# Performance work log

Hardware: AMD Instinct MI355X
Metric: run time of the kernel (lower is better)

The kernel has to match this reference:

```python
import jax, jax.numpy as jnp
import numpy as np

N_NODES = 10000
N_EDGES = 320000
IN_DIM = 128
HIDDEN = 256
NUM_LAYERS = 6
ALPHA = 0.1
LN_EPS = 1e-5


def setup_inputs() -> dict:
    key = jax.random.key(0)
    ks = jax.random.split(key, 12)
    x = jax.random.normal(ks[0], (N_NODES, IN_DIM), dtype=jnp.float32)
    edge_index = jax.random.randint(ks[1], (2, N_EDGES), 0, N_NODES, dtype=jnp.int64)
    # input MLP params
    W_in = jax.random.normal(ks[2], (IN_DIM, HIDDEN), dtype=jnp.float32) / np.sqrt(IN_DIM)
    b_in = jnp.zeros((HIDDEN,), dtype=jnp.float32)
    g_in = jnp.ones((HIDDEN,), dtype=jnp.float32)
    beta_in = jnp.zeros((HIDDEN,), dtype=jnp.float32)
    # per-layer GCNConv weight/bias + LayerNorm params, stacked over layers
    Wl = jax.random.normal(ks[3], (NUM_LAYERS, HIDDEN, HIDDEN), dtype=jnp.float32) / np.sqrt(HIDDEN)
    bl = jnp.zeros((NUM_LAYERS, HIDDEN), dtype=jnp.float32)
    gl = jnp.ones((NUM_LAYERS, HIDDEN), dtype=jnp.float32)
    betal = jnp.zeros((NUM_LAYERS, HIDDEN), dtype=jnp.float32)
    return {"x": x, "edge_index": edge_index, "W_in": W_in, "b_in": b_in,
            "g_in": g_in, "beta_in": beta_in, "Wl": Wl, "bl": bl,
            "gl": gl, "betal": betal}


def _layernorm(h, g, b):
    mu = jnp.mean(h, axis=-1, keepdims=True)
    var = jnp.var(h, axis=-1, keepdims=True)
    return (h - mu) * jax.lax.rsqrt(var + LN_EPS) * g + b


def reference(x, edge_index, W_in, b_in, g_in, beta_in, Wl, bl, gl, betal):
    N = x.shape[0]
    # input block: Linear -> GELU (exact erf) -> LayerNorm (dropout = eval identity)
    h = jax.nn.gelu(x @ W_in + b_in, approximate=False)
    h = _layernorm(h, g_in, beta_in)

    # GCN normalization with self loops, unit edge weights (edge_weight=None)
    loops = jnp.arange(N, dtype=edge_index.dtype)
    src = jnp.concatenate([edge_index[0], loops])  # [E+N] sources (j)
    dst = jnp.concatenate([edge_index[1], loops])  # [E+N] targets (i)
    w = jnp.ones((src.shape[0],), dtype=x.dtype)
    deg = jax.ops.segment_sum(w, dst, num_segments=N)
    dinv = jnp.where(deg > 0, deg ** -0.5, 0.0)
    norm = dinv[src] * w * dinv[dst]  # [E+N]

    h0 = h
    cur = h
    for l in range(NUM_LAYERS):
        m = cur @ Wl[l]                                        # [N,H] transform
        msgs = norm[:, None] * m[src]                          # gather + scale
        agg = jax.ops.segment_sum(msgs, dst, num_segments=N)   # scatter-add
        agg = agg + bl[l]
        hh = _layernorm(jax.nn.gelu(agg, approximate=False), gl[l], betal[l])
        cur = cur + (1.0 - ALPHA) * hh + ALPHA * h0
    return cur
```

## Files before the change

### kernel.cpp

```cpp
#include <hip/hip_runtime.h>
#include <math.h>

#define N_NODES   10000
#define N_EDGES   320000
#define IN_DIM    128
#define HIDDEN    256
#define NUM_LAYERS 6
#define ALPHA     0.1f
#define LN_EPS    1e-5f

__device__ __forceinline__ float gelu_exact(float x) {
    return 0.5f * x * (1.0f + erff(x * 0.70710678118654752440f));
}

__device__ __forceinline__ float wave_sum64(float v) {
#pragma unroll
    for (int i = 32; i > 0; i >>= 1) v += __shfl_xor(v, i);
    return v;
}


__global__ __launch_bounds__(256) void count_deg_kernel(const int* __restrict__ dst,
                                                        int* __restrict__ cnt) {
    int e = blockIdx.x * 256 + threadIdx.x;
    if (e < N_EDGES) atomicAdd(&cnt[dst[e]], 1);
}

__global__ __launch_bounds__(256) void dinv_kernel(const int* __restrict__ cnt,
                                                   float* __restrict__ dinv) {
    int i = blockIdx.x * 256 + threadIdx.x;
    if (i < N_NODES) dinv[i] = rsqrtf((float)(cnt[i] + 1));
}

__global__ __launch_bounds__(256) void scan_kernel(const int* __restrict__ cnt,
                                                   int* __restrict__ offs) {
    __shared__ int sums[256];
    __shared__ int bases[257];
    int t = threadIdx.x;
    const int chunk = (N_NODES + 255) / 256;
    int b0 = t * chunk;
    int b1 = b0 + chunk; if (b1 > N_NODES) b1 = N_NODES;
    if (b0 > N_NODES) b0 = N_NODES;
    int s = 0;
    for (int i = b0; i < b1; ++i) s += cnt[i];
    sums[t] = s;
    __syncthreads();
    if (t == 0) {
        int r = 0;
        for (int i = 0; i < 256; ++i) { bases[i] = r; r += sums[i]; }
        bases[256] = r;
    }
    __syncthreads();
    int r = bases[t];
    for (int i = b0; i < b1; ++i) { offs[i] = r; r += cnt[i]; }
    if (t == 0) offs[N_NODES] = bases[256];
}

__global__ __launch_bounds__(256) void fill_csr_kernel(const int* __restrict__ src,
                                                       const int* __restrict__ dst,
                                                       const float* __restrict__ dinv,
                                                       const int* __restrict__ offs,
                                                       int* __restrict__ cursor,
                                                       int* __restrict__ csr_src,
                                                       float* __restrict__ csr_norm) {
    int e = blockIdx.x * 256 + threadIdx.x;
    if (e < N_EDGES) {
        int d = dst[e], s = src[e];
        int pos = atomicAdd(&cursor[d], 1);
        int idx = offs[d] + pos;
        csr_src[idx]  = s;
        csr_norm[idx] = dinv[s] * dinv[d];
    }
}

template<int K>
__global__ __launch_bounds__(256) void gemm_kernel(const float* __restrict__ A,
                                                   const float* __restrict__ B,
                                                   float* __restrict__ C) {
    __shared__ float As[16][68];
    __shared__ float Bs[16][68];

    int tid = threadIdx.x;
    int tx = tid & 15;
    int ty = tid >> 4;
    int row0 = blockIdx.x * 64;
    int col0 = blockIdx.y * 64;

    float acc[4][4] = {};

    for (int k0 = 0; k0 < K; k0 += 16) {
        {
            int idx = tid * 4;
            int r  = idx >> 4;
            int kk = idx & 15;
            int row = row0 + r;
            if (row < N_NODES) {
                const float4 a4 = *(const float4*)&A[(size_t)row * K + k0 + kk];
                As[kk + 0][r] = a4.x; As[kk + 1][r] = a4.y;
                As[kk + 2][r] = a4.z; As[kk + 3][r] = a4.w;
            } else {
                As[kk + 0][r] = 0.f; As[kk + 1][r] = 0.f;
                As[kk + 2][r] = 0.f; As[kk + 3][r] = 0.f;
            }
        }
        {
            int idx = tid * 4;
            int rb = idx >> 6;
            int cb = idx & 63;
            const float4 b4 = *(const float4*)&B[(size_t)(k0 + rb) * HIDDEN + col0 + cb];
            *(float4*)&Bs[rb][cb] = b4;
        }
        __syncthreads();

        #pragma unroll
        for (int kk = 0; kk < 16; ++kk) {
            const float4 a4 = *(const float4*)&As[kk][ty * 4];
            const float4 b4 = *(const float4*)&Bs[kk][tx * 4];
            acc[0][0] += a4.x * b4.x; acc[0][1] += a4.x * b4.y; acc[0][2] += a4.x * b4.z; acc[0][3] += a4.x * b4.w;
            acc[1][0] += a4.y * b4.x; acc[1][1] += a4.y * b4.y; acc[1][2] += a4.y * b4.z; acc[1][3] += a4.y * b4.w;
            acc[2][0] += a4.z * b4.x; acc[2][1] += a4.z * b4.y; acc[2][2] += a4.z * b4.z; acc[2][3] += a4.z * b4.w;
            acc[3][0] += a4.w * b4.x; acc[3][1] += a4.w * b4.y; acc[3][2] += a4.w * b4.z; acc[3][3] += a4.w * b4.w;
        }
        __syncthreads();
    }

    #pragma unroll
    for (int i = 0; i < 4; ++i) {
        int row = row0 + ty * 4 + i;
        if (row < N_NODES) {
            float4 v = make_float4(acc[i][0], acc[i][1], acc[i][2], acc[i][3]);
            *(float4*)&C[(size_t)row * HIDDEN + col0 + tx * 4] = v;
        }
    }
}

__global__ __launch_bounds__(256) void ln_in_kernel(const float4* __restrict__ pre,
                                                    const float4* __restrict__ b4,
                                                    const float4* __restrict__ g4,
                                                    const float4* __restrict__ beta4,
                                                    float4* __restrict__ h0,
                                                    float4* __restrict__ cur) {
    int n = blockIdx.x * 4 + (threadIdx.x >> 6);
    int lane = threadIdx.x & 63;
    if (n >= N_NODES) return;

    float4 v = pre[(size_t)n * 64 + lane];
    float4 bb = b4[lane];
    float x0 = gelu_exact(v.x + bb.x);
    float x1 = gelu_exact(v.y + bb.y);
    float x2 = gelu_exact(v.z + bb.z);
    float x3 = gelu_exact(v.w + bb.w);

    float mu = wave_sum64(x0 + x1 + x2 + x3) * (1.0f / 256.0f);
    float d0 = x0 - mu, d1 = x1 - mu, d2 = x2 - mu, d3 = x3 - mu;
    float var = wave_sum64(d0 * d0 + d1 * d1 + d2 * d2 + d3 * d3) * (1.0f / 256.0f);
    float r = rsqrtf(var + LN_EPS);

    float4 gg = g4[lane], be = beta4[lane];
    float4 out = make_float4(d0 * r * gg.x + be.x, d1 * r * gg.y + be.y,
                             d2 * r * gg.z + be.z, d3 * r * gg.w + be.w);
    h0[(size_t)n * 64 + lane]  = out;
    cur[(size_t)n * 64 + lane] = out;
}

__global__ __launch_bounds__(256) void agg_fused_kernel(const float4* __restrict__ m4,
                                                        const float* __restrict__ dinv,
                                                        const int* __restrict__ offs,
                                                        const int* __restrict__ csr_src,
                                                        const float* __restrict__ csr_norm,
                                                        const float4* __restrict__ bias4,
                                                        const float4* __restrict__ g4,
                                                        const float4* __restrict__ beta4,
                                                        const float4* __restrict__ h04,
                                                        float4* __restrict__ cur4) {
    int n = blockIdx.x * 4 + (threadIdx.x >> 6);
    int lane = threadIdx.x & 63;
    if (n >= N_NODES) return;

    float dn = dinv[n];
    float dn2 = dn * dn;
    float4 sv = m4[(size_t)n * 64 + lane];
    float ax = sv.x * dn2, ay = sv.y * dn2, az = sv.z * dn2, aw = sv.w * dn2;

    int e  = offs[n];
    int e1 = offs[n + 1];
    for (; e + 7 < e1; e += 8) {
        int   s0 = csr_src[e + 0], s1 = csr_src[e + 1], s2 = csr_src[e + 2], s3 = csr_src[e + 3];
        int   s4 = csr_src[e + 4], s5 = csr_src[e + 5], s6 = csr_src[e + 6], s7 = csr_src[e + 7];
        float w0 = csr_norm[e + 0], w1 = csr_norm[e + 1], w2 = csr_norm[e + 2], w3 = csr_norm[e + 3];
        float w4 = csr_norm[e + 4], w5 = csr_norm[e + 5], w6 = csr_norm[e + 6], w7 = csr_norm[e + 7];
        float4 v0 = m4[(size_t)s0 * 64 + lane];
        float4 v1 = m4[(size_t)s1 * 64 + lane];
        float4 v2 = m4[(size_t)s2 * 64 + lane];
        float4 v3 = m4[(size_t)s3 * 64 + lane];
        float4 v4 = m4[(size_t)s4 * 64 + lane];
        float4 v5 = m4[(size_t)s5 * 64 + lane];
        float4 v6 = m4[(size_t)s6 * 64 + lane];
        float4 v7 = m4[(size_t)s7 * 64 + lane];
        ax += w0 * v0.x + w1 * v1.x + w2 * v2.x + w3 * v3.x;
        ay += w0 * v0.y + w1 * v1.y + w2 * v2.y + w3 * v3.y;
        az += w0 * v0.z + w1 * v1.z + w2 * v2.z + w3 * v3.z;
        aw += w0 * v0.w + w1 * v1.w + w2 * v2.w + w3 * v3.w;
        ax += w4 * v4.x + w5 * v5.x + w6 * v6.x + w7 * v7.x;
        ay += w4 * v4.y + w5 * v5.y + w6 * v6.y + w7 * v7.y;
        az += w4 * v4.z + w5 * v5.z + w6 * v6.z + w7 * v7.z;
        aw += w4 * v4.w + w5 * v5.w + w6 * v6.w + w7 * v7.w;
    }
    for (; e < e1; ++e) {
        int s = csr_src[e];
        float w = csr_norm[e];
        float4 vv = m4[(size_t)s * 64 + lane];
        ax += w * vv.x; ay += w * vv.y; az += w * vv.z; aw += w * vv.w;
    }

    float4 bb = bias4[lane];
    float x0 = gelu_exact(ax + bb.x);
    float x1 = gelu_exact(ay + bb.y);
    float x2 = gelu_exact(az + bb.z);
    float x3 = gelu_exact(aw + bb.w);

    float mu = wave_sum64(x0 + x1 + x2 + x3) * (1.0f / 256.0f);
    float d0 = x0 - mu, d1 = x1 - mu, d2 = x2 - mu, d3 = x3 - mu;
    float var = wave_sum64(d0 * d0 + d1 * d1 + d2 * d2 + d3 * d3) * (1.0f / 256.0f);
    float r = rsqrtf(var + LN_EPS);

    float4 gg = g4[lane], be = beta4[lane];
    float h0v = d0 * r * gg.x + be.x;
    float h1v = d1 * r * gg.y + be.y;
    float h2v = d2 * r * gg.z + be.z;
    float h3v = d3 * r * gg.w + be.w;

    size_t idx = (size_t)n * 64 + lane;
    float4 c = cur4[idx];
    float4 h = h04[idx];
    float4 o = make_float4(c.x + (1.0f - ALPHA) * h0v + ALPHA * h.x,
                           c.y + (1.0f - ALPHA) * h1v + ALPHA * h.y,
                           c.z + (1.0f - ALPHA) * h2v + ALPHA * h.z,
                           c.w + (1.0f - ALPHA) * h3v + ALPHA * h.w);
    cur4[idx] = o;
}


extern "C" void kernel_launch(void* const* d_in, const int* in_sizes, int n_in,
                              void* d_out, int out_size, void* d_ws, size_t ws_size,
                              hipStream_t stream) {
    const float* x      = (const float*)d_in[0];
    const int*   ei     = (const int*)  d_in[1];
    const float* W_in   = (const float*)d_in[2];
    const float* b_in   = (const float*)d_in[3];
    const float* g_in   = (const float*)d_in[4];
    const float* bt_in  = (const float*)d_in[5];
    const float* Wl     = (const float*)d_in[6];
    const float* bl     = (const float*)d_in[7];
    const float* gl     = (const float*)d_in[8];
    const float* betal  = (const float*)d_in[9];

    const int* src = ei;
    const int* dst = ei + N_EDGES;

    float* cur = (float*)d_out;

    char* w = (char*)d_ws;
    size_t off = 0;
    auto alloc = [&](size_t bytes) -> void* {
        void* p = w + off;
        off = (off + bytes + 255) & ~(size_t)255;
        return p;
    };
    int*   cnt      = (int*)  alloc(N_NODES * sizeof(int));
    int*   cursor   = (int*)  alloc(N_NODES * sizeof(int));
    int*   offs     = (int*)  alloc((N_NODES + 1) * sizeof(int));
    float* dinv     = (float*)alloc(N_NODES * sizeof(float));
    int*   csr_src  = (int*)  alloc(N_EDGES * sizeof(int));
    float* csr_norm = (float*)alloc(N_EDGES * sizeof(float));
    float* h0       = (float*)alloc((size_t)N_NODES * HIDDEN * sizeof(float));
    float* m        = (float*)alloc((size_t)N_NODES * HIDDEN * sizeof(float));

    hipMemsetAsync(cnt,    0, N_NODES * sizeof(int), stream);
    hipMemsetAsync(cursor, 0, N_NODES * sizeof(int), stream);

    const int EB = (N_EDGES + 255) / 256;
    const int NB = (N_NODES + 255) / 256;
    const int NODE_BLOCKS = (N_NODES + 3) / 4;

    count_deg_kernel<<<EB, 256, 0, stream>>>(dst, cnt);
    dinv_kernel<<<NB, 256, 0, stream>>>(cnt, dinv);
    scan_kernel<<<1, 256, 0, stream>>>(cnt, offs);
    fill_csr_kernel<<<EB, 256, 0, stream>>>(src, dst, dinv, offs, cursor, csr_src, csr_norm);

    dim3 ggrid((N_NODES + 63) / 64, HIDDEN / 64);

    gemm_kernel<IN_DIM><<<ggrid, 256, 0, stream>>>(x, W_in, m);
    ln_in_kernel<<<NODE_BLOCKS, 256, 0, stream>>>((const float4*)m, (const float4*)b_in,
                                                  (const float4*)g_in, (const float4*)bt_in,
                                                  (float4*)h0, (float4*)cur);

    for (int l = 0; l < NUM_LAYERS; ++l) {
        gemm_kernel<HIDDEN><<<ggrid, 256, 0, stream>>>(cur, Wl + (size_t)l * HIDDEN * HIDDEN, m);
        agg_fused_kernel<<<NODE_BLOCKS, 256, 0, stream>>>((const float4*)m, dinv, offs,
                                                          csr_src, csr_norm,
                                                          (const float4*)(bl + l * HIDDEN),
                                                          (const float4*)(gl + l * HIDDEN),
                                                          (const float4*)(betal + l * HIDDEN),
                                                          (const float4*)h0, (float4*)cur);
    }
}
```

Measured before the change: 558.6 us.

## Split aggregation into column-quarter gather kernel plus separate LN-residual kernel

New measurement: 578.9 us. 1.04x slower.

```diff
diff --git a/kernel.cpp b/kernel.cpp
--- a/kernel.cpp
+++ b/kernel.cpp
@@ -58,18 +58,14 @@
 
 __global__ __launch_bounds__(256) void fill_csr_kernel(const int* __restrict__ src,
                                                        const int* __restrict__ dst,
-                                                       const float* __restrict__ dinv,
                                                        const int* __restrict__ offs,
                                                        int* __restrict__ cursor,
-                                                       int* __restrict__ csr_src,
-                                                       float* __restrict__ csr_norm) {
+                                                       int* __restrict__ csr_src) {
     int e = blockIdx.x * 256 + threadIdx.x;
     if (e < N_EDGES) {
         int d = dst[e], s = src[e];
         int pos = atomicAdd(&cursor[d], 1);
-        int idx = offs[d] + pos;
-        csr_src[idx]  = s;
-        csr_norm[idx] = dinv[s] * dinv[d];
+        csr_src[offs[d] + pos] = s;
     }
 }
 
@@ -163,61 +159,62 @@
     cur[(size_t)n * 64 + lane] = out;
 }
 
-__global__ __launch_bounds__(256) void agg_fused_kernel(const float4* __restrict__ m4,
-                                                        const float* __restrict__ dinv,
-                                                        const int* __restrict__ offs,
-                                                        const int* __restrict__ csr_src,
-                                                        const float* __restrict__ csr_norm,
-                                                        const float4* __restrict__ bias4,
-                                                        const float4* __restrict__ g4,
-                                                        const float4* __restrict__ beta4,
-                                                        const float4* __restrict__ h04,
-                                                        float4* __restrict__ cur4) {
+__global__ __launch_bounds__(256) void gather_q_kernel(const float* __restrict__ m,
+                                                       const float* __restrict__ dinv,
+                                                       const int* __restrict__ offs,
+                                                       const int* __restrict__ csr_src,
+                                                       const float* __restrict__ bias,
+                                                       float* __restrict__ pre) {
+    int i  = blockIdx.x;
+    int q  = (i & 7) >> 1;
+    int nb = (i >> 3) * 2 + (i & 1);
+    int n  = nb * 4 + (threadIdx.x >> 6);
+    int lane = threadIdx.x & 63;
+    int col = q * 64 + lane;
+
+    float dn = dinv[n];
+    float acc = m[(size_t)n * HIDDEN + col] * (dn * dn);
+
+    int e  = offs[n];
+    int e1 = offs[n + 1];
+    for (; e + 7 < e1; e += 8) {
+        int s0 = csr_src[e + 0], s1 = csr_src[e + 1], s2 = csr_src[e + 2], s3 = csr_src[e + 3];
+        int s4 = csr_src[e + 4], s5 = csr_src[e + 5], s6 = csr_src[e + 6], s7 = csr_src[e + 7];
+        float v0 = m[(size_t)s0 * HIDDEN + col];
+        float v1 = m[(size_t)s1 * HIDDEN + col];
+        float v2 = m[(size_t)s2 * HIDDEN + col];
+        float v3 = m[(size_t)s3 * HIDDEN + col];
+        float v4 = m[(size_t)s4 * HIDDEN + col];
+        float v5 = m[(size_t)s5 * HIDDEN + col];
+        float v6 = m[(size_t)s6 * HIDDEN + col];
+        float v7 = m[(size_t)s7 * HIDDEN + col];
+        float w0 = dinv[s0] * dn, w1 = dinv[s1] * dn, w2 = dinv[s2] * dn, w3 = dinv[s3] * dn;
+        float w4 = dinv[s4] * dn, w5 = dinv[s5] * dn, w6 = dinv[s6] * dn, w7 = dinv[s7] * dn;
+        acc += w0 * v0 + w1 * v1 + w2 * v2 + w3 * v3;
+        acc += w4 * v4 + w5 * v5 + w6 * v6 + w7 * v7;
+    }
+    for (; e < e1; ++e) {
+        int s = csr_src[e];
+        acc += dinv[s] * dn * m[(size_t)s * HIDDEN + col];
+    }
+
+    pre[(size_t)n * HIDDEN + col] = acc + bias[col];
+}
+
+__global__ __launch_bounds__(256) void ln_res_kernel(const float4* __restrict__ pre4,
+                                                     const float4* __restrict__ g4,
+                                                     const float4* __restrict__ beta4,
+                                                     const float4* __restrict__ h04,
+                                                     float4* __restrict__ cur4) {
     int n = blockIdx.x * 4 + (threadIdx.x >> 6);
     int lane = threadIdx.x & 63;
     if (n >= N_NODES) return;
 
-    float dn = dinv[n];
-    float dn2 = dn * dn;
-    float4 sv = m4[(size_t)n * 64 + lane];
-    float ax = sv.x * dn2, ay = sv.y * dn2, az = sv.z * dn2, aw = sv.w * dn2;
-
-    int e  = offs[n];
-    int e1 = offs[n + 1];
-    for (; e + 7 < e1; e += 8) {
-        int   s0 = csr_src[e + 0], s1 = csr_src[e + 1], s2 = csr_src[e + 2], s3 = csr_src[e + 3];
-        int   s4 = csr_src[e + 4], s5 = csr_src[e + 5], s6 = csr_src[e + 6], s7 = csr_src[e + 7];
-        float w0 = csr_norm[e + 0], w1 = csr_norm[e + 1], w2 = csr_norm[e + 2], w3 = csr_norm[e + 3];
-        float w4 = csr_norm[e + 4], w5 = csr_norm[e + 5], w6 = csr_norm[e + 6], w7 = csr_norm[e + 7];
-        float4 v0 = m4[(size_t)s0 * 64 + lane];
-        float4 v1 = m4[(size_t)s1 * 64 + lane];
-        float4 v2 = m4[(size_t)s2 * 64 + lane];
-        float4 v3 = m4[(size_t)s3 * 64 + lane];
-        float4 v4 = m4[(size_t)s4 * 64 + lane];
-        float4 v5 = m4[(size_t)s5 * 64 + lane];
-        float4 v6 = m4[(size_t)s6 * 64 + lane];
-        float4 v7 = m4[(size_t)s7 * 64 + lane];
-        ax += w0 * v0.x + w1 * v1.x + w2 * v2.x + w3 * v3.x;
-        ay += w0 * v0.y + w1 * v1.y + w2 * v2.y + w3 * v3.y;
-        az += w0 * v0.z + w1 * v1.z + w2 * v2.z + w3 * v3.z;
-        aw += w0 * v0.w + w1 * v1.w + w2 * v2.w + w3 * v3.w;
-        ax += w4 * v4.x + w5 * v5.x + w6 * v6.x + w7 * v7.x;
-        ay += w4 * v4.y + w5 * v5.y + w6 * v6.y + w7 * v7.y;
-        az += w4 * v4.z + w5 * v5.z + w6 * v6.z + w7 * v7.z;
-        aw += w4 * v4.w + w5 * v5.w + w6 * v6.w + w7 * v7.w;
-    }
-    for (; e < e1; ++e) {
-        int s = csr_src[e];
-        float w = csr_norm[e];
-        float4 vv = m4[(size_t)s * 64 + lane];
-        ax += w * vv.x; ay += w * vv.y; az += w * vv.z; aw += w * vv.w;
-    }
-
-    float4 bb = bias4[lane];
-    float x0 = gelu_exact(ax + bb.x);
-    float x1 = gelu_exact(ay + bb.y);
-    float x2 = gelu_exact(az + bb.z);
-    float x3 = gelu_exact(aw + bb.w);
+    float4 v = pre4[(size_t)n * 64 + lane];
+    float x0 = gelu_exact(v.x);
+    float x1 = gelu_exact(v.y);
+    float x2 = gelu_exact(v.z);
+    float x3 = gelu_exact(v.w);
 
     float mu = wave_sum64(x0 + x1 + x2 + x3) * (1.0f / 256.0f);
     float d0 = x0 - mu, d1 = x1 - mu, d2 = x2 - mu, d3 = x3 - mu;
@@ -272,9 +269,9 @@
     int*   offs     = (int*)  alloc((N_NODES + 1) * sizeof(int));
     float* dinv     = (float*)alloc(N_NODES * sizeof(float));
     int*   csr_src  = (int*)  alloc(N_EDGES * sizeof(int));
-    float* csr_norm = (float*)alloc(N_EDGES * sizeof(float));
     float* h0       = (float*)alloc((size_t)N_NODES * HIDDEN * sizeof(float));
     float* m        = (float*)alloc((size_t)N_NODES * HIDDEN * sizeof(float));
+    float* pre      = (float*)alloc((size_t)N_NODES * HIDDEN * sizeof(float));
 
     hipMemsetAsync(cnt,    0, N_NODES * sizeof(int), stream);
     hipMemsetAsync(cursor, 0, N_NODES * sizeof(int), stream);
@@ -286,7 +283,7 @@
     count_deg_kernel<<<EB, 256, 0, stream>>>(dst, cnt);
     dinv_kernel<<<NB, 256, 0, stream>>>(cnt, dinv);
     scan_kernel<<<1, 256, 0, stream>>>(cnt, offs);
-    fill_csr_kernel<<<EB, 256, 0, stream>>>(src, dst, dinv, offs, cursor, csr_src, csr_norm);
+    fill_csr_kernel<<<EB, 256, 0, stream>>>(src, dst, offs, cursor, csr_src);
 
     dim3 ggrid((N_NODES + 63) / 64, HIDDEN / 64);
 
@@ -297,11 +294,11 @@
 
     for (int l = 0; l < NUM_LAYERS; ++l) {
         gemm_kernel<HIDDEN><<<ggrid, 256, 0, stream>>>(cur, Wl + (size_t)l * HIDDEN * HIDDEN, m);
-        agg_fused_kernel<<<NODE_BLOCKS, 256, 0, stream>>>((const float4*)m, dinv, offs,
-                                                          csr_src, csr_norm,
-                                                          (const float4*)(bl + l * HIDDEN),
-                                                          (const float4*)(gl + l * HIDDEN),
-                                                          (const float4*)(betal + l * HIDDEN),
-                                                          (const float4*)h0, (float4*)cur);
-    }
-}
+        gather_q_kernel<<<NODE_BLOCKS * 4, 256, 0, stream>>>(m, dinv, offs, csr_src,
+                                                             bl + l * HIDDEN, pre);
+        ln_res_kernel<<<NODE_BLOCKS, 256, 0, stream>>>((const float4*)pre,
+                                                       (const float4*)(gl + l * HIDDEN),
+                                                       (const float4*)(betal + l * HIDDEN),
+                                                       (const float4*)h0, (float4*)cur);
+    }
+}
```
